# Optimization experiments

Measured on AMD Instinct MI355X. Metric: run time of the kernel, lower is better.

## Reference

```python
import jax, jax.numpy as jnp
import numpy as np

H = 2048      # hidden_size
F = 1408      # moe_intermediate_size
E = 8         # num_experts
K = 2         # num_activated_experts
B, S = 4, 1024


def setup_inputs() -> dict:
    key = jax.random.key(0)
    ks = jax.random.split(key, 9)
    sc = 0.02
    return {
        "hidden_states": jax.random.normal(ks[0], (B, S, H), dtype=jnp.float32),
        "gate_w": jax.random.normal(ks[1], (E, H), dtype=jnp.float32) * sc,
        "bias": jnp.zeros((E,), dtype=jnp.float32),
        # shared expert (num_shared_experts = 1); torch Linear weight layout [out, in]
        "ws1": jax.random.normal(ks[2], (F, H), dtype=jnp.float32) * sc,
        "ws2": jax.random.normal(ks[3], (H, F), dtype=jnp.float32) * sc,
        "ws3": jax.random.normal(ks[4], (F, H), dtype=jnp.float32) * sc,
        # routed experts stacked along leading E axis
        "we1": jax.random.normal(ks[5], (E, F, H), dtype=jnp.float32) * sc,
        "we2": jax.random.normal(ks[6], (E, H, F), dtype=jnp.float32) * sc,
        "we3": jax.random.normal(ks[7], (E, F, H), dtype=jnp.float32) * sc,
    }


def reference(hidden_states, gate_w, bias, ws1, ws2, ws3, we1, we2, we3):
    orig_shape = hidden_states.shape
    x = hidden_states.reshape(-1, orig_shape[-1])      # [T, H]
    T = x.shape[0]

    # shared expert (SwiGLU)
    shared = (jax.nn.silu(x @ ws1.T) * (x @ ws3.T)) @ ws2.T   # [T, H]

    # sigmoid gating with bias-adjusted top-k selection
    scores = jax.nn.sigmoid(x @ gate_w.T)              # [T, E]
    routing_scores = scores + bias
    _, topk_idx = jax.lax.top_k(routing_scores, K)     # [T, K]
    sel = jnp.take_along_axis(scores, topk_idx, axis=1)
    gates = sel / sel.sum(axis=-1, keepdims=True)      # [T, K]

    # dense combine weights c[t, e] (top-k indices are distinct per token)
    c = jnp.zeros((T, E), dtype=x.dtype).at[jnp.arange(T)[:, None], topk_idx].add(gates)

    # all-expert SwiGLU, combined with sparse gate weights
    h1 = jnp.einsum("th,efh->etf", x, we1)             # [E, T, F]
    h3 = jnp.einsum("th,efh->etf", x, we3)
    act = jax.nn.silu(h1) * h3
    routed = jnp.einsum("etf,ehf,te->th", act, we2, c) # [T, H]

    return (shared + routed).reshape(orig_shape)
```

## Files before the change

### kernel.cpp

```cpp
#include <hip/hip_runtime.h>
#include <cstdint>
#include <cstddef>

#define TDIM 4096
#define HDIM 2048
#define FDIM 1408
#define NEXP 8
#define NSLOT (TDIM * 2)

typedef _Float16 half8 __attribute__((ext_vector_type(8)));
typedef float floatx4 __attribute__((ext_vector_type(4)));

#define AS1 __attribute__((address_space(1)))
#define AS3 __attribute__((address_space(3)))

__device__ __forceinline__ void g2l16(const _Float16* g, _Float16* l) {
  __builtin_amdgcn_global_load_lds((const AS1 unsigned*)g, (AS3 unsigned*)l, 16, 0, 0);
}

static constexpr size_t ws_align(size_t x) { return (x + 511) & ~(size_t)511; }
static constexpr size_t WS_XB     = 0;
static constexpr size_t WS_ACT_S  = WS_XB    + (size_t)TDIM * HDIM * 2;
static constexpr size_t WS_ACT_R  = WS_ACT_S + (size_t)TDIM * FDIM * 2;
static constexpr size_t WS_TOKE   = WS_ACT_R + (size_t)NSLOT * FDIM * 2;
static constexpr size_t WS_TOKG   = WS_TOKE  + (size_t)TDIM * 2 * 4;
static constexpr size_t WS_SLOTT  = WS_TOKG  + (size_t)TDIM * 2 * 4;
static constexpr size_t WS_SLOTG  = WS_SLOTT + (size_t)NSLOT * 4;
static constexpr size_t WS_COUNTS = WS_SLOTG + (size_t)NSLOT * 4;
static constexpr size_t WS_FILL   = WS_COUNTS + 64;
static constexpr size_t WS_OFFS   = WS_FILL   + 64;
static constexpr size_t WS_WS1H   = ws_align(WS_OFFS + 64);
static constexpr size_t WS_WS3H   = WS_WS1H + (size_t)FDIM * HDIM * 2;
static constexpr size_t WS_WS2H   = WS_WS3H + (size_t)FDIM * HDIM * 2;
static constexpr size_t WS_WE1H   = WS_WS2H + (size_t)HDIM * FDIM * 2;
static constexpr size_t WS_WE3H   = WS_WE1H + (size_t)NEXP * FDIM * HDIM * 2;
static constexpr size_t WS_WE2H   = WS_WE3H + (size_t)NEXP * FDIM * HDIM * 2;
static constexpr size_t WS_END    = WS_WE2H + (size_t)NEXP * HDIM * FDIM * 2;


__global__ void zero_meta_kernel(int* __restrict__ counts) {
  if (threadIdx.x < 32) counts[threadIdx.x] = 0;
}

__global__ void cvt_kernel(const float* __restrict__ src, _Float16* __restrict__ dst) {
  size_t i = ((size_t)blockIdx.x * 256 + threadIdx.x) * 8;
  float4 a = *(const float4*)(src + i);
  float4 b = *(const float4*)(src + i + 4);
  half8 h;
  h[0] = (_Float16)a.x; h[1] = (_Float16)a.y; h[2] = (_Float16)a.z; h[3] = (_Float16)a.w;
  h[4] = (_Float16)b.x; h[5] = (_Float16)b.y; h[6] = (_Float16)b.z; h[7] = (_Float16)b.w;
  *(half8*)(dst + i) = h;
}

__global__ void gate_kernel(const float* __restrict__ x, const float* __restrict__ gw,
                            const float* __restrict__ bias, int* __restrict__ toke,
                            float* __restrict__ tokg, int* __restrict__ counts) {
  const int wid  = blockIdx.x * 4 + (threadIdx.x >> 6);
  const int lane = threadIdx.x & 63;
  const float4* xv = (const float4*)(x + (size_t)wid * HDIM);
  const float4* gv = (const float4*)gw;
  float acc[NEXP];
#pragma unroll
  for (int e = 0; e < NEXP; ++e) acc[e] = 0.f;
#pragma unroll
  for (int i = 0; i < 8; ++i) {
    float4 xq = xv[lane + 64 * i];
#pragma unroll
    for (int e = 0; e < NEXP; ++e) {
      float4 gq = gv[e * 512 + lane + 64 * i];
      acc[e] += xq.x * gq.x + xq.y * gq.y + xq.z * gq.z + xq.w * gq.w;
    }
  }
#pragma unroll
  for (int e = 0; e < NEXP; ++e) {
    float v = acc[e];
    for (int off = 32; off; off >>= 1) v += __shfl_xor(v, off);
    acc[e] = v;
  }
  if (lane == 0) {
    float s[NEXP], r[NEXP];
#pragma unroll
    for (int e = 0; e < NEXP; ++e) {
      s[e] = 1.f / (1.f + __expf(-acc[e]));
      r[e] = s[e] + bias[e];
    }
    int e0 = 0;
#pragma unroll
    for (int e = 1; e < NEXP; ++e) if (r[e] > r[e0]) e0 = e;
    int e1 = -1;
#pragma unroll
    for (int e = 0; e < NEXP; ++e) if (e != e0 && (e1 < 0 || r[e] > r[e1])) e1 = e;
    float g0 = s[e0], g1 = s[e1];
    float inv = 1.f / (g0 + g1);
    toke[wid * 2]     = e0;
    toke[wid * 2 + 1] = e1;
    tokg[wid * 2]     = g0 * inv;
    tokg[wid * 2 + 1] = g1 * inv;
    atomicAdd(&counts[e0], 1);
    atomicAdd(&counts[e1], 1);
  }
}

__global__ void offsets_kernel(const int* __restrict__ counts, int* __restrict__ offs) {
  if (threadIdx.x == 0) {
    int o = 0;
    for (int e = 0; e < NEXP; ++e) { offs[e] = o; o += counts[e]; }
  }
}

__global__ void scatter_kernel(const int* __restrict__ toke, const float* __restrict__ tokg,
                               const int* __restrict__ offs, int* __restrict__ fill,
                               int* __restrict__ slott, float* __restrict__ slotg) {
  int t = blockIdx.x * 256 + threadIdx.x;
#pragma unroll
  for (int j = 0; j < 2; ++j) {
    int e = toke[t * 2 + j];
    float g = tokg[t * 2 + j];
    int p = offs[e] + atomicAdd(&fill[e], 1);
    slott[p] = t;
    slotg[p] = g;
  }
}


template <bool GATHER>
__global__ __launch_bounds__(256) void up_kernel(
    const _Float16* __restrict__ xb, const _Float16* __restrict__ w1g,
    const _Float16* __restrict__ w3g, _Float16* __restrict__ act,
    const int* __restrict__ counts, const int* __restrict__ offs,
    const int* __restrict__ slott) {
  int cnt = TDIM, base = 0, e = 0;
  if constexpr (GATHER) {
    e = blockIdx.z;
    cnt = counts[e];
    base = offs[e];
    if ((int)(blockIdx.y * 128) >= cnt) return;
  }
  const int m0 = blockIdx.y * 128, n0 = blockIdx.x * 128;
  const _Float16* __restrict__ W1 = w1g + (size_t)e * FDIM * HDIM;
  const _Float16* __restrict__ W3 = w3g + (size_t)e * FDIM * HDIM;

  __shared__ _Float16 As[128 * 64];
  __shared__ _Float16 B1s[128 * 64];
  __shared__ _Float16 B3s[128 * 64];

  const int tid = threadIdx.x, lane = tid & 63, wave = tid >> 6;
  const int wm = wave >> 1, wn = wave & 1;
  const int lrow = lane & 15, quad = lane >> 4;
  const int subrow = lane >> 3, cb = lane & 7;
  const int scb = (cb ^ subrow) * 8;

  const _Float16 *gA[4], *gB1[4], *gB3[4];
#pragma unroll
  for (int it = 0; it < 4; ++it) {
    int r = (it * 4 + wave) * 8 + subrow;
    int m = m0 + r;
    int tok;
    if constexpr (GATHER) tok = slott[base + (m < cnt ? m : cnt - 1)];
    else tok = m;
    gA[it]  = xb + (size_t)tok * HDIM + scb;
    gB1[it] = W1 + (size_t)(n0 + r) * HDIM + scb;
    gB3[it] = W3 + (size_t)(n0 + r) * HDIM + scb;
  }

  floatx4 acc1[4][4] = {};
  floatx4 acc3[4][4] = {};
  const int s = lrow & 7;

  for (int k0 = 0; k0 < HDIM; k0 += 64) {
#pragma unroll
    for (int it = 0; it < 4; ++it) {
      const int lb = (it * 4 + wave) * 512;
      g2l16(gA[it] + k0,  &As[lb]);
      g2l16(gB1[it] + k0, &B1s[lb]);
      g2l16(gB3[it] + k0, &B3s[lb]);
    }
    __syncthreads();
#pragma unroll
    for (int kk = 0; kk < 64; kk += 32) {
      const int cb0 = (kk >> 3) + quad;
      const int co = (cb0 ^ s) * 8;
      half8 af[4], b1f[4], b3f[4];
#pragma unroll
      for (int i = 0; i < 4; ++i)
        af[i] = *(const half8*)&As[(wm * 64 + i * 16 + lrow) * 64 + co];
#pragma unroll
      for (int i = 0; i < 4; ++i) {
        b1f[i] = *(const half8*)&B1s[(wn * 64 + i * 16 + lrow) * 64 + co];
        b3f[i] = *(const half8*)&B3s[(wn * 64 + i * 16 + lrow) * 64 + co];
      }
#pragma unroll
      for (int ms = 0; ms < 4; ++ms)
#pragma unroll
        for (int ns = 0; ns < 4; ++ns) {
          acc1[ms][ns] = __builtin_amdgcn_mfma_f32_16x16x32_f16(af[ms], b1f[ns], acc1[ms][ns], 0, 0, 0);
          acc3[ms][ns] = __builtin_amdgcn_mfma_f32_16x16x32_f16(af[ms], b3f[ns], acc3[ms][ns], 0, 0, 0);
        }
    }
    __syncthreads();
  }

#pragma unroll
  for (int ms = 0; ms < 4; ++ms)
#pragma unroll
    for (int ns = 0; ns < 4; ++ns)
#pragma unroll
      for (int r = 0; r < 4; ++r) {
        float h1 = acc1[ms][ns][r];
        float h3 = acc3[ms][ns][r];
        float a = h1 / (1.f + __expf(-h1)) * h3;
        int rl = wm * 64 + ms * 16 + quad * 4 + r;
        int f = n0 + wn * 64 + ns * 16 + lrow;
        int m = m0 + rl;
        if constexpr (GATHER) {
          if (m < cnt) act[(size_t)(base + m) * FDIM + f] = (_Float16)a;
        } else {
          act[(size_t)m * FDIM + f] = (_Float16)a;
        }
      }
}

template <bool GATHER>
__global__ __launch_bounds__(256) void down_kernel(
    const _Float16* __restrict__ act, const _Float16* __restrict__ w2g,
    float* __restrict__ out, const int* __restrict__ counts,
    const int* __restrict__ offs, const int* __restrict__ slott,
    const float* __restrict__ slotg) {
  int cnt = TDIM, base = 0, e = 0;
  if constexpr (GATHER) {
    e = blockIdx.z;
    cnt = counts[e];
    base = offs[e];
    if ((int)(blockIdx.y * 128) >= cnt) return;
  }
  const int m0 = blockIdx.y * 128, n0 = blockIdx.x * 128;
  const _Float16* __restrict__ W = w2g + (size_t)e * HDIM * FDIM;

  __shared__ _Float16 As[128 * 64];
  __shared__ _Float16 Bs[128 * 64];

  const int tid = threadIdx.x, lane = tid & 63, wave = tid >> 6;
  const int wm = wave >> 1, wn = wave & 1;
  const int lrow = lane & 15, quad = lane >> 4;
  const int subrow = lane >> 3, cb = lane & 7;
  const int scb = (cb ^ subrow) * 8;

  const _Float16 *gA[4], *gB[4];
#pragma unroll
  for (int it = 0; it < 4; ++it) {
    int r = (it * 4 + wave) * 8 + subrow;
    int m = m0 + r;
    int src;
    if constexpr (GATHER) src = base + (m < cnt ? m : cnt - 1);
    else src = m;
    gA[it] = act + (size_t)src * FDIM + scb;
    gB[it] = W + (size_t)(n0 + r) * FDIM + scb;
  }

  floatx4 acc[4][4] = {};
  const int s = lrow & 7;

  for (int k0 = 0; k0 < FDIM; k0 += 64) {
#pragma unroll
    for (int it = 0; it < 4; ++it) {
      const int lb = (it * 4 + wave) * 512;
      g2l16(gA[it] + k0, &As[lb]);
      g2l16(gB[it] + k0, &Bs[lb]);
    }
    __syncthreads();
#pragma unroll
    for (int kk = 0; kk < 64; kk += 32) {
      const int cb0 = (kk >> 3) + quad;
      const int co = (cb0 ^ s) * 8;
      half8 af[4], bf[4];
#pragma unroll
      for (int i = 0; i < 4; ++i)
        af[i] = *(const half8*)&As[(wm * 64 + i * 16 + lrow) * 64 + co];
#pragma unroll
      for (int i = 0; i < 4; ++i)
        bf[i] = *(const half8*)&Bs[(wn * 64 + i * 16 + lrow) * 64 + co];
#pragma unroll
      for (int ms = 0; ms < 4; ++ms)
#pragma unroll
        for (int ns = 0; ns < 4; ++ns)
          acc[ms][ns] = __builtin_amdgcn_mfma_f32_16x16x32_f16(af[ms], bf[ns], acc[ms][ns], 0, 0, 0);
    }
    __syncthreads();
  }

#pragma unroll
  for (int ms = 0; ms < 4; ++ms)
#pragma unroll
    for (int ns = 0; ns < 4; ++ns)
#pragma unroll
      for (int r = 0; r < 4; ++r) {
        float v = acc[ms][ns][r];
        int rl = wm * 64 + ms * 16 + quad * 4 + r;
        int h = n0 + wn * 64 + ns * 16 + lrow;
        int m = m0 + rl;
        if constexpr (GATHER) {
          if (m < cnt) {
            int slot = base + m;
            atomicAdd(&out[(size_t)slott[slot] * HDIM + h], v * slotg[slot]);
          }
        } else {
          out[(size_t)m * HDIM + h] = v;
        }
      }
}


extern "C" void kernel_launch(void* const* d_in, const int* in_sizes, int n_in,
                              void* d_out, int out_size, void* d_ws, size_t ws_size,
                              hipStream_t stream) {
  const float* x    = (const float*)d_in[0];
  const float* gw   = (const float*)d_in[1];
  const float* bias = (const float*)d_in[2];
  const float* ws1  = (const float*)d_in[3];
  const float* ws2  = (const float*)d_in[4];
  const float* ws3  = (const float*)d_in[5];
  const float* we1  = (const float*)d_in[6];
  const float* we2  = (const float*)d_in[7];
  const float* we3  = (const float*)d_in[8];
  float* out = (float*)d_out;

  char* ws = (char*)d_ws;
  _Float16* xb   = (_Float16*)(ws + WS_XB);
  _Float16* acts = (_Float16*)(ws + WS_ACT_S);
  _Float16* actr = (_Float16*)(ws + WS_ACT_R);
  int*   toke  = (int*)(ws + WS_TOKE);
  float* tokg  = (float*)(ws + WS_TOKG);
  int*   slott = (int*)(ws + WS_SLOTT);
  float* slotg = (float*)(ws + WS_SLOTG);
  int* counts  = (int*)(ws + WS_COUNTS);
  int* fill    = (int*)(ws + WS_FILL);
  int* offs    = (int*)(ws + WS_OFFS);
  _Float16* ws1h = (_Float16*)(ws + WS_WS1H);
  _Float16* ws3h = (_Float16*)(ws + WS_WS3H);
  _Float16* ws2h = (_Float16*)(ws + WS_WS2H);
  _Float16* we1h = (_Float16*)(ws + WS_WE1H);
  _Float16* we3h = (_Float16*)(ws + WS_WE3H);
  _Float16* we2h = (_Float16*)(ws + WS_WE2H);

  hipLaunchKernelGGL(zero_meta_kernel, dim3(1), dim3(64), 0, stream, counts);
  hipLaunchKernelGGL(cvt_kernel, dim3(4096), dim3(256), 0, stream, x, xb);
  hipLaunchKernelGGL(gate_kernel, dim3(1024), dim3(256), 0, stream, x, gw, bias, toke, tokg, counts);
  hipLaunchKernelGGL(offsets_kernel, dim3(1), dim3(64), 0, stream, counts, offs);
  hipLaunchKernelGGL(scatter_kernel, dim3(16), dim3(256), 0, stream, toke, tokg, offs, fill, slott, slotg);

  constexpr int GS = (FDIM * HDIM) / 2048;
  constexpr int GR = (NEXP * FDIM * HDIM) / 2048;
  hipLaunchKernelGGL(cvt_kernel, dim3(GS), dim3(256), 0, stream, ws1, ws1h);
  hipLaunchKernelGGL(cvt_kernel, dim3(GS), dim3(256), 0, stream, ws3, ws3h);
  hipLaunchKernelGGL(cvt_kernel, dim3(GS), dim3(256), 0, stream, ws2, ws2h);
  hipLaunchKernelGGL(cvt_kernel, dim3(GR), dim3(256), 0, stream, we1, we1h);
  hipLaunchKernelGGL(cvt_kernel, dim3(GR), dim3(256), 0, stream, we3, we3h);
  hipLaunchKernelGGL(cvt_kernel, dim3(GR), dim3(256), 0, stream, we2, we2h);

  hipLaunchKernelGGL((up_kernel<false>), dim3(FDIM / 128, TDIM / 128, 1), dim3(256), 0, stream,
                     xb, ws1h, ws3h, acts, nullptr, nullptr, nullptr);
  hipLaunchKernelGGL((up_kernel<true>), dim3(FDIM / 128, TDIM / 128, NEXP), dim3(256), 0, stream,
                     xb, we1h, we3h, actr, counts, offs, slott);
  hipLaunchKernelGGL((down_kernel<false>), dim3(HDIM / 128, TDIM / 128, 1), dim3(256), 0, stream,
                     acts, ws2h, out, nullptr, nullptr, nullptr, nullptr);
  hipLaunchKernelGGL((down_kernel<true>), dim3(HDIM / 128, TDIM / 128, NEXP), dim3(256), 0, stream,
                     actr, we2h, out, counts, offs, slott, slotg);
}
```

Before: 1.036 ms.

## Double-buffer GEMM tiles, merge shared/routed launches, fuse conversions into fewer kernels

The up and down GEMMs now use BK=32 tiles in two LDS buffers, so the next tile is prefetched while MFMAs run on the current one, with a new XOR swizzle. Shared and routed expert GEMMs are merged into one launch each through an extra grid z-slice. Weight conversions are batched three per launch and the x-to-fp16 conversion is folded into the gate kernel. The output is memset and the shared down-projection now uses atomics, which adds atomic traffic and a memset pass but removes the ordering dependency between the shared and routed down launches.

```diff
diff --git a/kernel.cpp b/kernel.cpp
--- a/kernel.cpp
+++ b/kernel.cpp
@@ -7,8 +7,10 @@
 #define FDIM 1408
 #define NEXP 8
 #define NSLOT (TDIM * 2)
+#define BK 32
 
 typedef _Float16 half8 __attribute__((ext_vector_type(8)));
+typedef _Float16 half4 __attribute__((ext_vector_type(4)));
 typedef float floatx4 __attribute__((ext_vector_type(4)));
 
 #define AS1 __attribute__((address_space(1)))
@@ -42,29 +44,42 @@
   if (threadIdx.x < 32) counts[threadIdx.x] = 0;
 }
 
-__global__ void cvt_kernel(const float* __restrict__ src, _Float16* __restrict__ dst) {
+__global__ void cvt3_kernel(const float* __restrict__ s0, const float* __restrict__ s1,
+                            const float* __restrict__ s2, _Float16* __restrict__ d0,
+                            _Float16* __restrict__ d1, _Float16* __restrict__ d2) {
+  const float* s;
+  _Float16* d;
+  if (blockIdx.y == 0)      { s = s0; d = d0; }
+  else if (blockIdx.y == 1) { s = s1; d = d1; }
+  else                      { s = s2; d = d2; }
   size_t i = ((size_t)blockIdx.x * 256 + threadIdx.x) * 8;
-  float4 a = *(const float4*)(src + i);
-  float4 b = *(const float4*)(src + i + 4);
+  float4 a = *(const float4*)(s + i);
+  float4 b = *(const float4*)(s + i + 4);
   half8 h;
   h[0] = (_Float16)a.x; h[1] = (_Float16)a.y; h[2] = (_Float16)a.z; h[3] = (_Float16)a.w;
   h[4] = (_Float16)b.x; h[5] = (_Float16)b.y; h[6] = (_Float16)b.z; h[7] = (_Float16)b.w;
-  *(half8*)(dst + i) = h;
+  *(half8*)(d + i) = h;
 }
 
 __global__ void gate_kernel(const float* __restrict__ x, const float* __restrict__ gw,
-                            const float* __restrict__ bias, int* __restrict__ toke,
-                            float* __restrict__ tokg, int* __restrict__ counts) {
+                            const float* __restrict__ bias, _Float16* __restrict__ xb,
+                            int* __restrict__ toke, float* __restrict__ tokg,
+                            int* __restrict__ counts) {
   const int wid  = blockIdx.x * 4 + (threadIdx.x >> 6);
   const int lane = threadIdx.x & 63;
   const float4* xv = (const float4*)(x + (size_t)wid * HDIM);
   const float4* gv = (const float4*)gw;
+  _Float16* xrow = xb + (size_t)wid * HDIM;
   float acc[NEXP];
 #pragma unroll
   for (int e = 0; e < NEXP; ++e) acc[e] = 0.f;
 #pragma unroll
   for (int i = 0; i < 8; ++i) {
     float4 xq = xv[lane + 64 * i];
+    half4 hq;
+    hq[0] = (_Float16)xq.x; hq[1] = (_Float16)xq.y;
+    hq[2] = (_Float16)xq.z; hq[3] = (_Float16)xq.w;
+    *(half4*)(xrow + 4 * (lane + 64 * i)) = hq;
 #pragma unroll
     for (int e = 0; e < NEXP; ++e) {
       float4 gq = gv[e * 512 + lane + 64 * i];
@@ -123,80 +138,94 @@
 }
 
 
-template <bool GATHER>
 __global__ __launch_bounds__(256) void up_kernel(
-    const _Float16* __restrict__ xb, const _Float16* __restrict__ w1g,
-    const _Float16* __restrict__ w3g, _Float16* __restrict__ act,
+    const _Float16* __restrict__ xb,
+    const _Float16* __restrict__ ws1h, const _Float16* __restrict__ ws3h,
+    const _Float16* __restrict__ we1h, const _Float16* __restrict__ we3h,
+    _Float16* __restrict__ acts, _Float16* __restrict__ actr,
     const int* __restrict__ counts, const int* __restrict__ offs,
     const int* __restrict__ slott) {
-  int cnt = TDIM, base = 0, e = 0;
-  if constexpr (GATHER) {
-    e = blockIdx.z;
+  const int z = blockIdx.z;
+  int cnt = TDIM, base = 0;
+  const _Float16* __restrict__ W1 = ws1h;
+  const _Float16* __restrict__ W3 = ws3h;
+  _Float16* __restrict__ act = acts;
+  bool gather = false;
+  if (z > 0) {
+    const int e = z - 1;
     cnt = counts[e];
     base = offs[e];
     if ((int)(blockIdx.y * 128) >= cnt) return;
+    W1 = we1h + (size_t)e * FDIM * HDIM;
+    W3 = we3h + (size_t)e * FDIM * HDIM;
+    act = actr;
+    gather = true;
   }
   const int m0 = blockIdx.y * 128, n0 = blockIdx.x * 128;
-  const _Float16* __restrict__ W1 = w1g + (size_t)e * FDIM * HDIM;
-  const _Float16* __restrict__ W3 = w3g + (size_t)e * FDIM * HDIM;
-
-  __shared__ _Float16 As[128 * 64];
-  __shared__ _Float16 B1s[128 * 64];
-  __shared__ _Float16 B3s[128 * 64];
-
-  const int tid = threadIdx.x, lane = tid & 63, wave = tid >> 6;
-  const int wm = wave >> 1, wn = wave & 1;
+
+  __shared__ _Float16 As[2][128 * BK];
+  __shared__ _Float16 B1s[2][128 * BK];
+  __shared__ _Float16 B3s[2][128 * BK];
+
+  const int tid = threadIdx.x, lane = tid & 63, wv = tid >> 6;
+  const int wm = wv >> 1, wn = wv & 1;
   const int lrow = lane & 15, quad = lane >> 4;
-  const int subrow = lane >> 3, cb = lane & 7;
-  const int scb = (cb ^ subrow) * 8;
-
-  const _Float16 *gA[4], *gB1[4], *gB3[4];
-#pragma unroll
-  for (int it = 0; it < 4; ++it) {
-    int r = (it * 4 + wave) * 8 + subrow;
-    int m = m0 + r;
+
+  const _Float16 *srcA[2], *srcB1[2], *srcB3[2];
+#pragma unroll
+  for (int j = 0; j < 2; ++j) {
+    const int rr = wv * 32 + j * 16 + (lane >> 2);
+    const int gc = ((lane & 3) ^ ((rr >> 1) & 3)) * 8;
+    const int m = m0 + rr;
     int tok;
-    if constexpr (GATHER) tok = slott[base + (m < cnt ? m : cnt - 1)];
+    if (gather) tok = slott[base + (m < cnt ? m : cnt - 1)];
     else tok = m;
-    gA[it]  = xb + (size_t)tok * HDIM + scb;
-    gB1[it] = W1 + (size_t)(n0 + r) * HDIM + scb;
-    gB3[it] = W3 + (size_t)(n0 + r) * HDIM + scb;
+    srcA[j]  = xb + (size_t)tok * HDIM + gc;
+    srcB1[j] = W1 + (size_t)(n0 + rr) * HDIM + gc;
+    srcB3[j] = W3 + (size_t)(n0 + rr) * HDIM + gc;
   }
 
   floatx4 acc1[4][4] = {};
   floatx4 acc3[4][4] = {};
-  const int s = lrow & 7;
-
-  for (int k0 = 0; k0 < HDIM; k0 += 64) {
-#pragma unroll
-    for (int it = 0; it < 4; ++it) {
-      const int lb = (it * 4 + wave) * 512;
-      g2l16(gA[it] + k0,  &As[lb]);
-      g2l16(gB1[it] + k0, &B1s[lb]);
-      g2l16(gB3[it] + k0, &B3s[lb]);
+  const int cA = (quad ^ ((lrow >> 1) & 3)) * 8;
+
+#pragma unroll
+  for (int j = 0; j < 2; ++j) {
+    const int lb = (wv * 32 + j * 16) * BK;
+    g2l16(srcA[j],  &As[0][lb]);
+    g2l16(srcB1[j], &B1s[0][lb]);
+    g2l16(srcB3[j], &B3s[0][lb]);
+  }
+  __syncthreads();
+
+  for (int t = 0; t < HDIM / BK; ++t) {
+    const int cur = t & 1;
+    if (t + 1 < HDIM / BK) {
+      const int k0 = (t + 1) * BK;
+#pragma unroll
+      for (int j = 0; j < 2; ++j) {
+        const int lb = (wv * 32 + j * 16) * BK;
+        g2l16(srcA[j] + k0,  &As[cur ^ 1][lb]);
+        g2l16(srcB1[j] + k0, &B1s[cur ^ 1][lb]);
+        g2l16(srcB3[j] + k0, &B3s[cur ^ 1][lb]);
+      }
     }
-    __syncthreads();
-#pragma unroll
-    for (int kk = 0; kk < 64; kk += 32) {
-      const int cb0 = (kk >> 3) + quad;
-      const int co = (cb0 ^ s) * 8;
-      half8 af[4], b1f[4], b3f[4];
-#pragma unroll
-      for (int i = 0; i < 4; ++i)
-        af[i] = *(const half8*)&As[(wm * 64 + i * 16 + lrow) * 64 + co];
-#pragma unroll
-      for (int i = 0; i < 4; ++i) {
-        b1f[i] = *(const half8*)&B1s[(wn * 64 + i * 16 + lrow) * 64 + co];
-        b3f[i] = *(const half8*)&B3s[(wn * 64 + i * 16 + lrow) * 64 + co];
+    half8 af[4], b1f[4], b3f[4];
+#pragma unroll
+    for (int i = 0; i < 4; ++i)
+      af[i] = *(const half8*)&As[cur][(wm * 64 + i * 16 + lrow) * BK + cA];
+#pragma unroll
+    for (int i = 0; i < 4; ++i) {
+      b1f[i] = *(const half8*)&B1s[cur][(wn * 64 + i * 16 + lrow) * BK + cA];
+      b3f[i] = *(const half8*)&B3s[cur][(wn * 64 + i * 16 + lrow) * BK + cA];
+    }
+#pragma unroll
+    for (int ms = 0; ms < 4; ++ms)
+#pragma unroll
+      for (int ns = 0; ns < 4; ++ns) {
+        acc1[ms][ns] = __builtin_amdgcn_mfma_f32_16x16x32_f16(af[ms], b1f[ns], acc1[ms][ns], 0, 0, 0);
+        acc3[ms][ns] = __builtin_amdgcn_mfma_f32_16x16x32_f16(af[ms], b3f[ns], acc3[ms][ns], 0, 0, 0);
       }
-#pragma unroll
-      for (int ms = 0; ms < 4; ++ms)
-#pragma unroll
-        for (int ns = 0; ns < 4; ++ns) {
-          acc1[ms][ns] = __builtin_amdgcn_mfma_f32_16x16x32_f16(af[ms], b1f[ns], acc1[ms][ns], 0, 0, 0);
-          acc3[ms][ns] = __builtin_amdgcn_mfma_f32_16x16x32_f16(af[ms], b3f[ns], acc3[ms][ns], 0, 0, 0);
-        }
-    }
     __syncthreads();
   }
 
@@ -209,10 +238,10 @@
         float h1 = acc1[ms][ns][r];
         float h3 = acc3[ms][ns][r];
         float a = h1 / (1.f + __expf(-h1)) * h3;
-        int rl = wm * 64 + ms * 16 + quad * 4 + r;
-        int f = n0 + wn * 64 + ns * 16 + lrow;
-        int m = m0 + rl;
-        if constexpr (GATHER) {
+        const int rl = wm * 64 + ms * 16 + quad * 4 + r;
+        const int f = n0 + wn * 64 + ns * 16 + lrow;
+        const int m = m0 + rl;
+        if (gather) {
           if (m < cnt) act[(size_t)(base + m) * FDIM + f] = (_Float16)a;
         } else {
           act[(size_t)m * FDIM + f] = (_Float16)a;
@@ -220,71 +249,82 @@
       }
 }
 
-template <bool GATHER>
 __global__ __launch_bounds__(256) void down_kernel(
-    const _Float16* __restrict__ act, const _Float16* __restrict__ w2g,
-    float* __restrict__ out, const int* __restrict__ counts,
-    const int* __restrict__ offs, const int* __restrict__ slott,
-    const float* __restrict__ slotg) {
-  int cnt = TDIM, base = 0, e = 0;
-  if constexpr (GATHER) {
-    e = blockIdx.z;
+    const _Float16* __restrict__ acts, const _Float16* __restrict__ actr,
+    const _Float16* __restrict__ ws2h, const _Float16* __restrict__ we2h,
+    float* __restrict__ out,
+    const int* __restrict__ counts, const int* __restrict__ offs,
+    const int* __restrict__ slott, const float* __restrict__ slotg) {
+  const int z = blockIdx.z;
+  int cnt = TDIM, base = 0;
+  const _Float16* __restrict__ A = acts;
+  const _Float16* __restrict__ W = ws2h;
+  bool gather = false;
+  if (z > 0) {
+    const int e = z - 1;
     cnt = counts[e];
     base = offs[e];
     if ((int)(blockIdx.y * 128) >= cnt) return;
+    A = actr;
+    W = we2h + (size_t)e * HDIM * FDIM;
+    gather = true;
   }
   const int m0 = blockIdx.y * 128, n0 = blockIdx.x * 128;
-  const _Float16* __restrict__ W = w2g + (size_t)e * HDIM * FDIM;
-
-  __shared__ _Float16 As[128 * 64];
-  __shared__ _Float16 Bs[128 * 64];
-
-  const int tid = threadIdx.x, lane = tid & 63, wave = tid >> 6;
-  const int wm = wave >> 1, wn = wave & 1;
+
+  __shared__ _Float16 As[2][128 * BK];
+  __shared__ _Float16 Bs[2][128 * BK];
+
+  const int tid = threadIdx.x, lane = tid & 63, wv = tid >> 6;
+  const int wm = wv >> 1, wn = wv & 1;
   const int lrow = lane & 15, quad = lane >> 4;
-  const int subrow = lane >> 3, cb = lane & 7;
-  const int scb = (cb ^ subrow) * 8;
-
-  const _Float16 *gA[4], *gB[4];
-#pragma unroll
-  for (int it = 0; it < 4; ++it) {
-    int r = (it * 4 + wave) * 8 + subrow;
-    int m = m0 + r;
-    int src;
-    if constexpr (GATHER) src = base + (m < cnt ? m : cnt - 1);
-    else src = m;
-    gA[it] = act + (size_t)src * FDIM + scb;
-    gB[it] = W + (size_t)(n0 + r) * FDIM + scb;
+
+  const _Float16 *srcA[2], *srcB[2];
+#pragma unroll
+  for (int j = 0; j < 2; ++j) {
+    const int rr = wv * 32 + j * 16 + (lane >> 2);
+    const int gc = ((lane & 3) ^ ((rr >> 1) & 3)) * 8;
+    const int m = m0 + rr;
+    int srow;
+    if (gather) srow = base + (m < cnt ? m : cnt - 1);
+    else srow = m;
+    srcA[j] = A + (size_t)srow * FDIM + gc;
+    srcB[j] = W + (size_t)(n0 + rr) * FDIM + gc;
   }
 
   floatx4 acc[4][4] = {};
-  const int s = lrow & 7;
-
-  for (int k0 = 0; k0 < FDIM; k0 += 64) {
-#pragma unroll
-    for (int it = 0; it < 4; ++it) {
-      const int lb = (it * 4 + wave) * 512;
-      g2l16(gA[it] + k0, &As[lb]);
-      g2l16(gB[it] + k0, &Bs[lb]);
+  const int cA = (quad ^ ((lrow >> 1) & 3)) * 8;
+
+#pragma unroll
+  for (int j = 0; j < 2; ++j) {
+    const int lb = (wv * 32 + j * 16) * BK;
+    g2l16(srcA[j], &As[0][lb]);
+    g2l16(srcB[j], &Bs[0][lb]);
+  }
+  __syncthreads();
+
+  for (int t = 0; t < FDIM / BK; ++t) {
+    const int cur = t & 1;
+    if (t + 1 < FDIM / BK) {
+      const int k0 = (t + 1) * BK;
+#pragma unroll
+      for (int j = 0; j < 2; ++j) {
+        const int lb = (wv * 32 + j * 16) * BK;
+        g2l16(srcA[j] + k0, &As[cur ^ 1][lb]);
+        g2l16(srcB[j] + k0, &Bs[cur ^ 1][lb]);
+      }
     }
-    __syncthreads();
-#pragma unroll
-    for (int kk = 0; kk < 64; kk += 32) {
-      const int cb0 = (kk >> 3) + quad;
-      const int co = (cb0 ^ s) * 8;
-      half8 af[4], bf[4];
-#pragma unroll
-      for (int i = 0; i < 4; ++i)
-        af[i] = *(const half8*)&As[(wm * 64 + i * 16 + lrow) * 64 + co];
-#pragma unroll
-      for (int i = 0; i < 4; ++i)
-        bf[i] = *(const half8*)&Bs[(wn * 64 + i * 16 + lrow) * 64 + co];
-#pragma unroll
-      for (int ms = 0; ms < 4; ++ms)
-#pragma unroll
-        for (int ns = 0; ns < 4; ++ns)
-          acc[ms][ns] = __builtin_amdgcn_mfma_f32_16x16x32_f16(af[ms], bf[ns], acc[ms][ns], 0, 0, 0);
-    }
+    half8 af[4], bf[4];
+#pragma unroll
+    for (int i = 0; i < 4; ++i)
+      af[i] = *(const half8*)&As[cur][(wm * 64 + i * 16 + lrow) * BK + cA];
+#pragma unroll
+    for (int i = 0; i < 4; ++i)
+      bf[i] = *(const half8*)&Bs[cur][(wn * 64 + i * 16 + lrow) * BK + cA];
+#pragma unroll
+    for (int ms = 0; ms < 4; ++ms)
+#pragma unroll
+      for (int ns = 0; ns < 4; ++ns)
+        acc[ms][ns] = __builtin_amdgcn_mfma_f32_16x16x32_f16(af[ms], bf[ns], acc[ms][ns], 0, 0, 0);
     __syncthreads();
   }
 
@@ -295,16 +335,16 @@
 #pragma unroll
       for (int r = 0; r < 4; ++r) {
         float v = acc[ms][ns][r];
-        int rl = wm * 64 + ms * 16 + quad * 4 + r;
-        int h = n0 + wn * 64 + ns * 16 + lrow;
-        int m = m0 + rl;
-        if constexpr (GATHER) {
+        const int rl = wm * 64 + ms * 16 + quad * 4 + r;
+        const int h = n0 + wn * 64 + ns * 16 + lrow;
+        const int m = m0 + rl;
+        if (gather) {
           if (m < cnt) {
-            int slot = base + m;
-            atomicAdd(&out[(size_t)slott[slot] * HDIM + h], v * slotg[slot]);
+            const int sl = base + m;
+            atomicAdd(&out[(size_t)slott[sl] * HDIM + h], v * slotg[sl]);
           }
         } else {
-          out[(size_t)m * HDIM + h] = v;
+          atomicAdd(&out[(size_t)m * HDIM + h], v);
         }
       }
 }
@@ -343,26 +383,19 @@
   _Float16* we2h = (_Float16*)(ws + WS_WE2H);
 
   hipLaunchKernelGGL(zero_meta_kernel, dim3(1), dim3(64), 0, stream, counts);
-  hipLaunchKernelGGL(cvt_kernel, dim3(4096), dim3(256), 0, stream, x, xb);
-  hipLaunchKernelGGL(gate_kernel, dim3(1024), dim3(256), 0, stream, x, gw, bias, toke, tokg, counts);
+  hipLaunchKernelGGL(gate_kernel, dim3(1024), dim3(256), 0, stream, x, gw, bias, xb, toke, tokg, counts);
   hipLaunchKernelGGL(offsets_kernel, dim3(1), dim3(64), 0, stream, counts, offs);
   hipLaunchKernelGGL(scatter_kernel, dim3(16), dim3(256), 0, stream, toke, tokg, offs, fill, slott, slotg);
 
   constexpr int GS = (FDIM * HDIM) / 2048;
   constexpr int GR = (NEXP * FDIM * HDIM) / 2048;
-  hipLaunchKernelGGL(cvt_kernel, dim3(GS), dim3(256), 0, stream, ws1, ws1h);
-  hipLaunchKernelGGL(cvt_kernel, dim3(GS), dim3(256), 0, stream, ws3, ws3h);
-  hipLaunchKernelGGL(cvt_kernel, dim3(GS), dim3(256), 0, stream, ws2, ws2h);
-  hipLaunchKernelGGL(cvt_kernel, dim3(GR), dim3(256), 0, stream, we1, we1h);
-  hipLaunchKernelGGL(cvt_kernel, dim3(GR), dim3(256), 0, stream, we3, we3h);
-  hipLaunchKernelGGL(cvt_kernel, dim3(GR), dim3(256), 0, stream, we2, we2h);
-
-  hipLaunchKernelGGL((up_kernel<false>), dim3(FDIM / 128, TDIM / 128, 1), dim3(256), 0, stream,
-                     xb, ws1h, ws3h, acts, nullptr, nullptr, nullptr);
-  hipLaunchKernelGGL((up_kernel<true>), dim3(FDIM / 128, TDIM / 128, NEXP), dim3(256), 0, stream,
-                     xb, we1h, we3h, actr, counts, offs, slott);
-  hipLaunchKernelGGL((down_kernel<false>), dim3(HDIM / 128, TDIM / 128, 1), dim3(256), 0, stream,
-                     acts, ws2h, out, nullptr, nullptr, nullptr, nullptr);
-  hipLaunchKernelGGL((down_kernel<true>), dim3(HDIM / 128, TDIM / 128, NEXP), dim3(256), 0, stream,
-                     actr, we2h, out, counts, offs, slott, slotg);
-}
+  hipLaunchKernelGGL(cvt3_kernel, dim3(GS, 3), dim3(256), 0, stream, ws1, ws3, ws2, ws1h, ws3h, ws2h);
+  hipLaunchKernelGGL(cvt3_kernel, dim3(GR, 3), dim3(256), 0, stream, we1, we3, we2, we1h, we3h, we2h);
+
+  hipMemsetAsync(out, 0, (size_t)TDIM * HDIM * sizeof(float), stream);
+
+  hipLaunchKernelGGL(up_kernel, dim3(FDIM / 128, TDIM / 128, NEXP + 1), dim3(256), 0, stream,
+                     xb, ws1h, ws3h, we1h, we3h, acts, actr, counts, offs, slott);
+  hipLaunchKernelGGL(down_kernel, dim3(HDIM / 128, TDIM / 128, NEXP + 1), dim3(256), 0, stream,
+                     acts, actr, ws2h, we2h, out, counts, offs, slott, slotg);
+}
```

Result: faster. 966.9 us (-6.7%).
